# Optimization experiments

Hardware: AMD Instinct MI355X
Metric: run time of the kernel (lower is better)

## Reference

```python
import jax, jax.numpy as jnp
import numpy as np

K = 10       # APPNP propagation steps
ALPHA = 0.1  # teleport probability (beta in configs)


def setup_inputs() -> dict:
    key = jax.random.key(0)
    ks = jax.random.split(key, 4)
    N, F, H, C, E = 100000, 500, 64, 40, 3200000
    x = jax.random.normal(ks[0], (N, F), dtype=jnp.float32)
    W1 = jax.random.normal(ks[1], (F, H), dtype=jnp.float32) * (1.0 / np.sqrt(F))
    b1 = jnp.zeros((H,), dtype=jnp.float32)
    W2 = jax.random.normal(ks[2], (H, C), dtype=jnp.float32) * (1.0 / np.sqrt(H))
    b2 = jnp.zeros((C,), dtype=jnp.float32)
    edge_index = jax.random.randint(ks[3], (2, E), 0, N, dtype=jnp.int64)
    return {"x": x, "W1": W1, "b1": b1, "W2": W2, "b2": b2, "edge_index": edge_index}


def reference(x, W1, b1, W2, b2, edge_index):
    N = x.shape[0]
    # MLP (dropout is identity in eval mode)
    h = jnp.maximum(x @ W1 + b1, 0.0)
    h = h @ W2 + b2
    # gcn_norm with self-loops (PyG APPNP default): A_hat = D^-1/2 (A+I) D^-1/2
    loop = jnp.arange(N, dtype=edge_index.dtype)
    src = jnp.concatenate([edge_index[0], loop])  # message sources (x_j)
    dst = jnp.concatenate([edge_index[1], loop])  # aggregation targets
    deg = jax.ops.segment_sum(jnp.ones(src.shape[0], h.dtype), dst, num_segments=N)
    dinv = jnp.where(deg > 0, jax.lax.rsqrt(jnp.maximum(deg, 1.0)), 0.0)
    norm = dinv[src] * dinv[dst]  # [E+N]
    # K-step personalized-PageRank propagation: h <- (1-a) A_hat h + a h0
    h0 = h
    for _ in range(K):
        msg = h[src] * norm[:, None]                         # gather + scale
        agg = jax.ops.segment_sum(msg, dst, num_segments=N)  # scatter-add
        h = (1.0 - ALPHA) * agg + ALPHA * h0
    return jax.nn.log_softmax(h, axis=1)
```

## Files before the change

### kernel.cpp

```cpp
#include <hip/hip_runtime.h>
#include <math.h>

#define F_IN   500
#define H_DIM  64
#define C_DIM  40
#define K_STEPS 10
#define ALPHA  0.1f

typedef float vf4 __attribute__((ext_vector_type(4)));
typedef _Float16 hf;
typedef _Float16 h4 __attribute__((ext_vector_type(4)));

#define LDA1 68
__global__ __launch_bounds__(256) void mlp_gemm(
    const float* __restrict__ x, const float* __restrict__ W1,
    const float* __restrict__ b1, const float* __restrict__ W2,
    const float* __restrict__ b2, float* __restrict__ h0,
    hf* __restrict__ hA, int N)
{
    __shared__ float smem[64 * LDA1 * 2 + H_DIM * C_DIM];
    float* xs  = smem;
    float* ws  = smem + 64 * LDA1;
    float* w2s = smem + 2 * 64 * LDA1;

    const int t    = threadIdx.x;
    const int row0 = blockIdx.x * 64;
    const int tx   = t & 15;
    const int ty   = t >> 4;

    for (int i = t; i < H_DIM * C_DIM; i += 256) w2s[i] = W2[i];

    const float4 b1v = *(const float4*)&b1[tx * 4];

    float acc[4][4];
    #pragma unroll
    for (int i = 0; i < 4; ++i)
        #pragma unroll
        for (int j = 0; j < 4; ++j) acc[i][j] = 0.f;

    for (int k0 = 0; k0 < F_IN; k0 += 64) {
        __syncthreads();
        #pragma unroll
        for (int i = 0; i < 4; ++i) {
            int f  = t + i * 256;
            int r  = f >> 4;
            int c4 = (f & 15) << 2;
            int grow = row0 + r, gk = k0 + c4;
            float4 v = make_float4(0.f, 0.f, 0.f, 0.f);
            if (grow < N && gk < F_IN)
                v = *(const float4*)&x[(long long)grow * F_IN + gk];
            xs[(c4 + 0) * LDA1 + r] = v.x;
            xs[(c4 + 1) * LDA1 + r] = v.y;
            xs[(c4 + 2) * LDA1 + r] = v.z;
            xs[(c4 + 3) * LDA1 + r] = v.w;
        }
        #pragma unroll
        for (int i = 0; i < 4; ++i) {
            int f  = t + i * 256;
            int r  = f >> 4;
            int c4 = (f & 15) << 2;
            int gk = k0 + r;
            float4 v = make_float4(0.f, 0.f, 0.f, 0.f);
            if (gk < F_IN)
                v = *(const float4*)&W1[(long long)gk * H_DIM + c4];
            *(float4*)&ws[r * LDA1 + c4] = v;
        }
        __syncthreads();
        #pragma unroll 8
        for (int kk = 0; kk < 64; ++kk) {
            float4 a4 = *(const float4*)&xs[kk * LDA1 + ty * 4];
            float4 b4 = *(const float4*)&ws[kk * LDA1 + tx * 4];
            const float av[4] = {a4.x, a4.y, a4.z, a4.w};
            const float bv[4] = {b4.x, b4.y, b4.z, b4.w};
            #pragma unroll
            for (int i = 0; i < 4; ++i)
                #pragma unroll
                for (int j = 0; j < 4; ++j)
                    acc[i][j] = fmaf(av[i], bv[j], acc[i][j]);
        }
    }

    __syncthreads();
    #pragma unroll
    for (int i = 0; i < 4; ++i) {
        float4 hv;
        hv.x = fmaxf(acc[i][0] + b1v.x, 0.f);
        hv.y = fmaxf(acc[i][1] + b1v.y, 0.f);
        hv.z = fmaxf(acc[i][2] + b1v.z, 0.f);
        hv.w = fmaxf(acc[i][3] + b1v.w, 0.f);
        *(float4*)&xs[(ty * 4 + i) * LDA1 + tx * 4] = hv;
    }
    __syncthreads();

    for (int o = t; o < 64 * C_DIM; o += 256) {
        int r = o / C_DIM;
        int c = o - r * C_DIM;
        float s = b2[c];
        #pragma unroll 16
        for (int j = 0; j < H_DIM; ++j)
            s = fmaf(xs[r * LDA1 + j], w2s[j * C_DIM + c], s);
        int grow = row0 + r;
        if (grow < N) {
            long long idx = (long long)grow * C_DIM + c;
            h0[idx] = s;
            hA[idx] = (hf)s;
        }
    }
}

__global__ void deg_init(float* __restrict__ deg, int N) {
    int i = blockIdx.x * 256 + threadIdx.x;
    if (i < N) deg[i] = 1.0f;
}

__global__ void deg_count(const int* __restrict__ dst, float* __restrict__ deg, int E) {
    int e = blockIdx.x * 256 + threadIdx.x;
    if (e < E) atomicAdd(&deg[dst[e]], 1.0f);
}

__global__ void dinv_kernel(float* __restrict__ deg, int* __restrict__ lengths, int N) {
    int i = blockIdx.x * 256 + threadIdx.x;
    if (i < N) {
        float d = deg[i];
        deg[i] = 1.0f / sqrtf(d);
        lengths[i] = (int)(d - 0.5f);
    }
}

__global__ void scan1(const int* __restrict__ len, int* __restrict__ rp,
                      int* __restrict__ bsums, int N) {
    __shared__ int tmp[256];
    int tid = threadIdx.x;
    int gid = blockIdx.x * 256 + tid;
    int v = (gid < N) ? len[gid] : 0;
    tmp[tid] = v;
    __syncthreads();
    for (int off = 1; off < 256; off <<= 1) {
        int t = (tid >= off) ? tmp[tid - off] : 0;
        __syncthreads();
        tmp[tid] += t;
        __syncthreads();
    }
    if (gid < N) rp[gid] = tmp[tid] - v;
    if (tid == 255) bsums[blockIdx.x] = tmp[tid];
}

__global__ void scan2(int* __restrict__ bsums, int nb) {
    __shared__ int tmp[512];
    int tid = threadIdx.x;
    int v = (tid < nb) ? bsums[tid] : 0;
    tmp[tid] = v;
    __syncthreads();
    for (int off = 1; off < 512; off <<= 1) {
        int t = (tid >= off) ? tmp[tid - off] : 0;
        __syncthreads();
        tmp[tid] += t;
        __syncthreads();
    }
    if (tid < nb) bsums[tid] = tmp[tid] - v;
}

__global__ void scan3(int* __restrict__ rp, const int* __restrict__ bsums,
                      int* __restrict__ cursor, int N, int E) {
    int gid = blockIdx.x * 256 + threadIdx.x;
    if (gid < N) {
        int v = rp[gid] + bsums[blockIdx.x];
        rp[gid] = v;
        cursor[gid] = v;
    }
    if (gid == 0) rp[N] = E;
}

__global__ void csr_fill_direct(const int* __restrict__ src, const int* __restrict__ dst,
                                const float* __restrict__ dinv,
                                int* __restrict__ cursor, int* __restrict__ earr, int E) {
    int e = blockIdx.x * 256 + threadIdx.x;
    if (e >= E) return;
    int s = src[e];
    int d = dst[e];
    int pos = atomicAdd(&cursor[d], 1);
    unsigned wq = (unsigned)(dinv[s] * 32767.f + 0.5f);
    earr[pos] = (int)((unsigned)s | (wq << 17));
}

__global__ __launch_bounds__(256) void prop_h(
    const hf* __restrict__ hin, const float* __restrict__ h0,
    const float* __restrict__ dinv, const int* __restrict__ rp,
    const int* __restrict__ earr,
    hf* __restrict__ hout, int N)
{
    const int wave = threadIdx.x >> 6;
    const int lane = threadIdx.x & 63;
    const int row  = blockIdx.x * 4 + wave;
    if (row >= N) return;

    const int rs = rp[row];
    const int re = rp[row + 1];
    const float dr     = dinv[row];
    const float factor = (1.0f - ALPHA) * dr;
    const int e4 = lane >> 4;
    const int q  = lane & 15;
    const int qc = (q < 10) ? q : 9;

    const float invq = 1.0f / 32767.f;
    vf4 a0 = {0.f, 0.f, 0.f, 0.f};
    vf4 a1 = {0.f, 0.f, 0.f, 0.f};

    for (int base = rs; base < re; base += 64) {
        int ee = base + lane;
        int p = 0;
        if (ee < re) p = __builtin_nontemporal_load(&earr[ee]);
        int cnt = re - base; if (cnt > 64) cnt = 64;
        for (int i = 0; i < cnt; i += 8) {
            int p0 = __shfl(p, i + e4);
            int p1 = __shfl(p, i + 4 + e4);
            int   s0 = (int)((unsigned)p0 & 0x1FFFFu);
            int   s1 = (int)((unsigned)p1 & 0x1FFFFu);
            float w0 = (float)((unsigned)p0 >> 17) * invq;
            float w1 = (float)((unsigned)p1 >> 17) * invq;
            const h4 v0h = *(const h4*)(hin + (size_t)s0 * C_DIM + qc * 4);
            const h4 v1h = *(const h4*)(hin + (size_t)s1 * C_DIM + qc * 4);
            const vf4 v0 = __builtin_convertvector(v0h, vf4);
            const vf4 v1 = __builtin_convertvector(v1h, vf4);
            a0.x = fmaf(w0, v0.x, a0.x);
            a0.y = fmaf(w0, v0.y, a0.y);
            a0.z = fmaf(w0, v0.z, a0.z);
            a0.w = fmaf(w0, v0.w, a0.w);
            a1.x = fmaf(w1, v1.x, a1.x);
            a1.y = fmaf(w1, v1.y, a1.y);
            a1.z = fmaf(w1, v1.z, a1.z);
            a1.w = fmaf(w1, v1.w, a1.w);
        }
    }

    vf4 acc = a0 + a1;
    acc.x += __shfl_xor(acc.x, 16);
    acc.y += __shfl_xor(acc.y, 16);
    acc.z += __shfl_xor(acc.z, 16);
    acc.w += __shfl_xor(acc.w, 16);
    acc.x += __shfl_xor(acc.x, 32);
    acc.y += __shfl_xor(acc.y, 32);
    acc.z += __shfl_xor(acc.z, 32);
    acc.w += __shfl_xor(acc.w, 32);

    if (lane < 10) {
        const size_t rbase = (size_t)row * C_DIM + lane * 4;
        const h4 hvh = *(const h4*)(hin + rbase);
        const vf4 hv = __builtin_convertvector(hvh, vf4);
        const float4 h0v = *(const float4*)&h0[rbase];
        vf4 o;
        o.x = fmaf(factor, acc.x + dr * hv.x, ALPHA * h0v.x);
        o.y = fmaf(factor, acc.y + dr * hv.y, ALPHA * h0v.y);
        o.z = fmaf(factor, acc.z + dr * hv.z, ALPHA * h0v.z);
        o.w = fmaf(factor, acc.w + dr * hv.w, ALPHA * h0v.w);
        h4 oh;
        oh.x = (hf)o.x; oh.y = (hf)o.y; oh.z = (hf)o.z; oh.w = (hf)o.w;
        *(h4*)(hout + rbase) = oh;
    }
}

__global__ __launch_bounds__(256) void lsm_kernel(const hf* __restrict__ hin,
                                                  float* __restrict__ out, int N) {
    const int wave = threadIdx.x >> 6;
    const int lane = threadIdx.x & 63;
    const int row  = blockIdx.x * 4 + wave;
    if (row >= N) return;

    float v = (lane < C_DIM) ? (float)hin[(size_t)row * C_DIM + lane] : -INFINITY;
    float m = v;
    for (int off = 32; off; off >>= 1) m = fmaxf(m, __shfl_xor(m, off));
    float e = (lane < C_DIM) ? expf(v - m) : 0.f;
    float s = e;
    for (int off = 32; off; off >>= 1) s += __shfl_xor(s, off);
    if (lane < C_DIM) out[(long long)row * C_DIM + lane] = (v - m) - logf(s);
}

extern "C" void kernel_launch(void* const* d_in, const int* in_sizes, int n_in,
                              void* d_out, int out_size, void* d_ws, size_t ws_size,
                              hipStream_t stream) {
    const float* x  = (const float*)d_in[0];
    const float* W1 = (const float*)d_in[1];
    const float* b1 = (const float*)d_in[2];
    const float* W2 = (const float*)d_in[3];
    const float* b2 = (const float*)d_in[4];
    const int* ei = (const int*)d_in[5];

    const int N = in_sizes[0] / F_IN;
    const int E = in_sizes[5] / 2;
    const int* src = ei;
    const int* dst = ei + E;
    float* out = (float*)d_out;

    char* w = (char*)d_ws;
    float* h0    = (float*)w;  w += (size_t)N * C_DIM * 4;
    hf*    hA    = (hf*)w;     w += (size_t)N * C_DIM * 2;
    hf*    hB    = (hf*)w;     w += (size_t)N * C_DIM * 2;
    float* dinv  = (float*)w;  w += (size_t)N * 4;
    int*   rp    = (int*)w;    w += (size_t)(N + 1) * 4;
    int*   cursor= (int*)w;    w += (size_t)N * 4;
    int*   bsums = (int*)w;    w += (size_t)512 * 4;
    int*   earr  = (int*)w;    w += (size_t)E * 4;

    const int nbN = (N + 255) / 256;
    const int nbE = (E + 255) / 256;
    const int nbRow = (N + 3) / 4;
    const int nbGemm = (N + 63) / 64;

    mlp_gemm<<<nbGemm, 256, 0, stream>>>(x, W1, b1, W2, b2, h0, hA, N);

    deg_init <<<nbN, 256, 0, stream>>>(dinv, N);
    deg_count<<<nbE, 256, 0, stream>>>(dst, dinv, E);
    dinv_kernel<<<nbN, 256, 0, stream>>>(dinv, cursor, N);

    scan1<<<nbN, 256, 0, stream>>>(cursor, rp, bsums, N);
    scan2<<<1, 512, 0, stream>>>(bsums, nbN);
    scan3<<<nbN, 256, 0, stream>>>(rp, bsums, cursor, N, E);

    csr_fill_direct<<<nbE, 256, 0, stream>>>(src, dst, dinv, cursor, earr, E);

    hf* a = hA; hf* b = hB;
    for (int k = 0; k < K_STEPS; ++k) {
        prop_h<<<nbRow, 256, 0, stream>>>(a, h0, dinv, rp, earr, b, N);
        hf* t = a; a = b; b = t;
    }

    lsm_kernel<<<nbRow, 256, 0, stream>>>(a, out, N);
}
```

Baseline: 1.359 ms.

## Store propagated features as custom FP8 in 64-byte padded rows

Replaces the fp16 intermediate feature buffers with a hand-rolled 8-bit float format (fp16 bits scaled by 1/256 and truncated), stored in 64-byte aligned rows. This halves the bytes fetched by each random gather in the propagation steps, which are memory bound. The final step writes fp32 straight into the output buffer, and log-softmax then runs in place on it. The cost is much lower precision in the intermediate state across 10 steps, plus clamping at ±440, which risks accuracy failures.

New measurement: 1.379 ms. Within noise of the previous version (+1.5%).

```diff
diff --git a/kernel.cpp b/kernel.cpp
--- a/kernel.cpp
+++ b/kernel.cpp
@@ -6,17 +6,38 @@
 #define C_DIM  40
 #define K_STEPS 10
 #define ALPHA  0.1f
+#define ROWB   64
 
 typedef float vf4 __attribute__((ext_vector_type(4)));
-typedef _Float16 hf;
-typedef _Float16 h4 __attribute__((ext_vector_type(4)));
+typedef _Float16 h2 __attribute__((ext_vector_type(2)));
+
+__device__ __forceinline__ unsigned enc_fp8(float v) {
+    v = fminf(fmaxf(v, -440.f), 440.f);
+    _Float16 h = (_Float16)(v * (1.f / 256.f));
+    unsigned short u = __builtin_bit_cast(unsigned short, h);
+    unsigned mag = u & 0x7fffu;
+    unsigned r = (mag + 0x3Fu + ((mag >> 7) & 1u)) >> 7;
+    if (r > 127u) r = 127u;
+    return ((u >> 8) & 0x80u) | r;
+}
+
+__device__ __forceinline__ vf4 dec4(unsigned u) {
+    unsigned d02 = ((u & 0x007f007fu) << 7) | ((u & 0x00800080u) << 8);
+    unsigned v   = u >> 8;
+    unsigned d13 = ((v & 0x007f007fu) << 7) | ((v & 0x00800080u) << 8);
+    h2 a = __builtin_bit_cast(h2, d02);
+    h2 b = __builtin_bit_cast(h2, d13);
+    vf4 r;
+    r.x = (float)a.x; r.y = (float)b.x; r.z = (float)a.y; r.w = (float)b.y;
+    return r;
+}
 
 #define LDA1 68
 __global__ __launch_bounds__(256) void mlp_gemm(
     const float* __restrict__ x, const float* __restrict__ W1,
     const float* __restrict__ b1, const float* __restrict__ W2,
     const float* __restrict__ b2, float* __restrict__ h0,
-    hf* __restrict__ hA, int N)
+    unsigned char* __restrict__ hA8, int N)
 {
     __shared__ float smem[64 * LDA1 * 2 + H_DIM * C_DIM];
     float* xs  = smem;
@@ -101,9 +122,8 @@
             s = fmaf(xs[r * LDA1 + j], w2s[j * C_DIM + c], s);
         int grow = row0 + r;
         if (grow < N) {
-            long long idx = (long long)grow * C_DIM + c;
-            h0[idx] = s;
-            hA[idx] = (hf)s;
+            h0[(long long)grow * C_DIM + c] = s;
+            hA8[(size_t)grow * ROWB + c] = (unsigned char)enc_fp8(s);
         }
     }
 }
@@ -183,11 +203,11 @@
     earr[pos] = (int)((unsigned)s | (wq << 17));
 }
 
-__global__ __launch_bounds__(256) void prop_h(
-    const hf* __restrict__ hin, const float* __restrict__ h0,
+__global__ __launch_bounds__(256) void prop8(
+    const unsigned char* __restrict__ hin, const float* __restrict__ h0,
     const float* __restrict__ dinv, const int* __restrict__ rp,
     const int* __restrict__ earr,
-    hf* __restrict__ hout, int N)
+    unsigned char* __restrict__ hout, float* __restrict__ hout32, int N)
 {
     const int wave = threadIdx.x >> 6;
     const int lane = threadIdx.x & 63;
@@ -202,7 +222,7 @@
     const int q  = lane & 15;
     const int qc = (q < 10) ? q : 9;
 
-    const float invq = 1.0f / 32767.f;
+    const float invq256 = 256.f / 32767.f;
     vf4 a0 = {0.f, 0.f, 0.f, 0.f};
     vf4 a1 = {0.f, 0.f, 0.f, 0.f};
 
@@ -216,12 +236,12 @@
             int p1 = __shfl(p, i + 4 + e4);
             int   s0 = (int)((unsigned)p0 & 0x1FFFFu);
             int   s1 = (int)((unsigned)p1 & 0x1FFFFu);
-            float w0 = (float)((unsigned)p0 >> 17) * invq;
-            float w1 = (float)((unsigned)p1 >> 17) * invq;
-            const h4 v0h = *(const h4*)(hin + (size_t)s0 * C_DIM + qc * 4);
-            const h4 v1h = *(const h4*)(hin + (size_t)s1 * C_DIM + qc * 4);
-            const vf4 v0 = __builtin_convertvector(v0h, vf4);
-            const vf4 v1 = __builtin_convertvector(v1h, vf4);
+            float w0 = (float)((unsigned)p0 >> 17) * invq256;
+            float w1 = (float)((unsigned)p1 >> 17) * invq256;
+            const unsigned u0 = *(const unsigned*)(hin + ((size_t)s0 << 6) + (qc << 2));
+            const unsigned u1 = *(const unsigned*)(hin + ((size_t)s1 << 6) + (qc << 2));
+            const vf4 v0 = dec4(u0);
+            const vf4 v1 = dec4(u1);
             a0.x = fmaf(w0, v0.x, a0.x);
             a0.y = fmaf(w0, v0.y, a0.y);
             a0.z = fmaf(w0, v0.z, a0.z);
@@ -244,35 +264,39 @@
     acc.w += __shfl_xor(acc.w, 32);
 
     if (lane < 10) {
-        const size_t rbase = (size_t)row * C_DIM + lane * 4;
-        const h4 hvh = *(const h4*)(hin + rbase);
-        const vf4 hv = __builtin_convertvector(hvh, vf4);
-        const float4 h0v = *(const float4*)&h0[rbase];
+        const unsigned us = *(const unsigned*)(hin + ((size_t)row << 6) + (lane << 2));
+        const vf4 hv = dec4(us);
+        const float dr256 = dr * 256.f;
+        const float4 h0v = *(const float4*)&h0[(size_t)row * C_DIM + lane * 4];
         vf4 o;
-        o.x = fmaf(factor, acc.x + dr * hv.x, ALPHA * h0v.x);
-        o.y = fmaf(factor, acc.y + dr * hv.y, ALPHA * h0v.y);
-        o.z = fmaf(factor, acc.z + dr * hv.z, ALPHA * h0v.z);
-        o.w = fmaf(factor, acc.w + dr * hv.w, ALPHA * h0v.w);
-        h4 oh;
-        oh.x = (hf)o.x; oh.y = (hf)o.y; oh.z = (hf)o.z; oh.w = (hf)o.w;
-        *(h4*)(hout + rbase) = oh;
-    }
-}
-
-__global__ __launch_bounds__(256) void lsm_kernel(const hf* __restrict__ hin,
-                                                  float* __restrict__ out, int N) {
+        o.x = fmaf(factor, acc.x + dr256 * hv.x, ALPHA * h0v.x);
+        o.y = fmaf(factor, acc.y + dr256 * hv.y, ALPHA * h0v.y);
+        o.z = fmaf(factor, acc.z + dr256 * hv.z, ALPHA * h0v.z);
+        o.w = fmaf(factor, acc.w + dr256 * hv.w, ALPHA * h0v.w);
+        if (hout32) {
+            *(float4*)&hout32[(size_t)row * C_DIM + lane * 4] =
+                make_float4(o.x, o.y, o.z, o.w);
+        } else {
+            unsigned ob = enc_fp8(o.x) | (enc_fp8(o.y) << 8) |
+                          (enc_fp8(o.z) << 16) | (enc_fp8(o.w) << 24);
+            *(unsigned*)(hout + ((size_t)row << 6) + (lane << 2)) = ob;
+        }
+    }
+}
+
+__global__ __launch_bounds__(256) void lsm_kernel(float* __restrict__ buf, int N) {
     const int wave = threadIdx.x >> 6;
     const int lane = threadIdx.x & 63;
     const int row  = blockIdx.x * 4 + wave;
     if (row >= N) return;
 
-    float v = (lane < C_DIM) ? (float)hin[(size_t)row * C_DIM + lane] : -INFINITY;
+    float v = (lane < C_DIM) ? buf[(size_t)row * C_DIM + lane] : -INFINITY;
     float m = v;
     for (int off = 32; off; off >>= 1) m = fmaxf(m, __shfl_xor(m, off));
     float e = (lane < C_DIM) ? expf(v - m) : 0.f;
     float s = e;
     for (int off = 32; off; off >>= 1) s += __shfl_xor(s, off);
-    if (lane < C_DIM) out[(long long)row * C_DIM + lane] = (v - m) - logf(s);
+    if (lane < C_DIM) buf[(size_t)row * C_DIM + lane] = (v - m) - logf(s);
 }
 
 extern "C" void kernel_launch(void* const* d_in, const int* in_sizes, int n_in,
@@ -292,9 +316,9 @@
     float* out = (float*)d_out;
 
     char* w = (char*)d_ws;
-    float* h0    = (float*)w;  w += (size_t)N * C_DIM * 4;
-    hf*    hA    = (hf*)w;     w += (size_t)N * C_DIM * 2;
-    hf*    hB    = (hf*)w;     w += (size_t)N * C_DIM * 2;
+    float*         h0   = (float*)w;         w += (size_t)N * C_DIM * 4;
+    unsigned char* s8A  = (unsigned char*)w; w += (size_t)N * ROWB;
+    unsigned char* s8B  = (unsigned char*)w; w += (size_t)N * ROWB;
     float* dinv  = (float*)w;  w += (size_t)N * 4;
     int*   rp    = (int*)w;    w += (size_t)(N + 1) * 4;
     int*   cursor= (int*)w;    w += (size_t)N * 4;
@@ -306,7 +330,7 @@
     const int nbRow = (N + 3) / 4;
     const int nbGemm = (N + 63) / 64;
 
-    mlp_gemm<<<nbGemm, 256, 0, stream>>>(x, W1, b1, W2, b2, h0, hA, N);
+    mlp_gemm<<<nbGemm, 256, 0, stream>>>(x, W1, b1, W2, b2, h0, s8A, N);
 
     deg_init <<<nbN, 256, 0, stream>>>(dinv, N);
     deg_count<<<nbE, 256, 0, stream>>>(dst, dinv, E);
@@ -318,11 +342,14 @@
 
     csr_fill_direct<<<nbE, 256, 0, stream>>>(src, dst, dinv, cursor, earr, E);
 
-    hf* a = hA; hf* b = hB;
+    unsigned char* pa = s8A;
+    unsigned char* pb = s8B;
     for (int k = 0; k < K_STEPS; ++k) {
-        prop_h<<<nbRow, 256, 0, stream>>>(a, h0, dinv, rp, earr, b, N);
-        hf* t = a; a = b; b = t;
-    }
-
-    lsm_kernel<<<nbRow, 256, 0, stream>>>(a, out, N);
-}
+        const int last = (k == K_STEPS - 1);
+        prop8<<<nbRow, 256, 0, stream>>>(pa, h0, dinv, rp, earr,
+                                         pb, last ? out : nullptr, N);
+        unsigned char* t = pa; pa = pb; pb = t;
+    }
+
+    lsm_kernel<<<nbRow, 256, 0, stream>>>(out, N);
+}
```
